# Kernel optimization log

Hardware: AMD Instinct MI355X
Metric: run time of the kernel (lower is better)

Reference implementation:

```python
import jax, jax.numpy as jnp
import numpy as np

EPS = 1e-10

def _iou(a, b):
    """IoU for boxes in (cx, cy, w, h) format; a, b: (..., 4)."""
    a_min = a[..., :2] - a[..., 2:] * 0.5
    a_max = a[..., :2] + a[..., 2:] * 0.5
    b_min = b[..., :2] - b[..., 2:] * 0.5
    b_max = b[..., :2] + b[..., 2:] * 0.5
    inter_wh = jnp.clip(jnp.minimum(a_max, b_max) - jnp.maximum(a_min, b_min), 0.0)
    inter = inter_wh[..., 0] * inter_wh[..., 1]
    area_a = a[..., 2] * a[..., 3]
    area_b = b[..., 2] * b[..., 3]
    return inter / (area_a + area_b - inter + EPS)

def setup_inputs() -> dict:
    key = jax.random.key(0)
    k1, k2, k3 = jax.random.split(key, 3)
    BATCH, S, C = 16384, 7, 30
    # uniform in (0.01, 1) so sqrt() of w,h channels is finite/differentiable
    preds = jax.random.uniform(k1, (BATCH, S, S, C), jnp.float32, 0.01, 1.0)
    labels = jax.random.uniform(k2, (BATCH, S, S, C), jnp.float32, 0.01, 1.0)
    obj = jax.random.bernoulli(k3, 0.15, (BATCH, S, S)).astype(jnp.float32)
    labels = labels.at[..., 4].set(obj)  # code branches on labels[...,4] == 1
    return {"preds": preds, "labels": labels}

def reference(preds, labels):
    batch = preds.shape[0]
    obj = labels[..., 4] == 1.0  # (B, S, S)
    # faithful quirk: label bbox x-coord is read transposed (labels[i, y, x, 0])
    lb0 = jnp.swapaxes(labels[..., 0], 1, 2)
    lbox = jnp.stack([lb0, labels[..., 1], labels[..., 2], labels[..., 3]], axis=-1)
    iou1 = _iou(preds[..., 0:4], lbox)
    iou2 = _iou(preds[..., 5:9], lbox)
    choose1 = iou1 > iou2
    # branch where box 1 is responsible
    b1 = (5.0 * jnp.sum((preds[..., 0:2] - labels[..., 0:2]) ** 2, -1)
          + jnp.sum((jnp.sqrt(preds[..., 2:4]) - jnp.sqrt(labels[..., 2:4])) ** 2, -1)
          + (iou1 - preds[..., 4]) ** 2
          + 0.5 * preds[..., 9] ** 2)
    # branch where box 2 is responsible (targets read from labels[...,5:9] as in source)
    b2 = (5.0 * jnp.sum((preds[..., 5:7] - labels[..., 5:7]) ** 2, -1)
          + jnp.sum((jnp.sqrt(preds[..., 7:9]) - jnp.sqrt(labels[..., 7:9])) ** 2, -1)
          + (iou2 - preds[..., 9]) ** 2
          + 0.5 * preds[..., 4] ** 2)
    cls = jnp.sum((labels[..., 10:] - preds[..., 10:]) ** 2, -1)
    obj_loss = jnp.where(choose1, b1, b2) + cls
    noobj_loss = 0.5 * (preds[..., 4] ** 2 + preds[..., 9] ** 2)
    total = jnp.sum(jnp.where(obj, obj_loss, noobj_loss))
    return total / batch
```

## Files before the change

kernel.cpp:

```cpp
#include <hip/hip_runtime.h>


#define BATCH 16384
#define S 7
#define C 30
#define NCELLS (BATCH * S * S)
#define BLOCK 256
#define NC 256
#define NBLK (NCELLS / NC)
#define F4_PER_ARR (NC * C / 4)

#define GLOBAL_LOAD_LDS16(g, l)                                         \
    __builtin_amdgcn_global_load_lds(                                   \
        (const __attribute__((address_space(1))) void*)(g),             \
        (__attribute__((address_space(3))) void*)(l), 16, 0, 0)

__device__ __forceinline__ float sq(float v) { return v * v; }

__device__ __forceinline__ float iou_box(float acx, float acy, float aw, float ah,
                                         float bcx, float bcy, float bw, float bh) {
    float ax0 = acx - aw * 0.5f, ax1 = acx + aw * 0.5f;
    float ay0 = acy - ah * 0.5f, ay1 = acy + ah * 0.5f;
    float bx0 = bcx - bw * 0.5f, bx1 = bcx + bw * 0.5f;
    float by0 = bcy - bh * 0.5f, by1 = bcy + bh * 0.5f;
    float iw = fmaxf(fminf(ax1, bx1) - fmaxf(ax0, bx0), 0.0f);
    float ih = fmaxf(fminf(ay1, by1) - fmaxf(ay0, by0), 0.0f);
    float inter = iw * ih;
    float denom = aw * ah + bw * bh - inter + 1e-10f;
    return inter / denom;
}

__global__ __launch_bounds__(BLOCK) void yolo_partial_kernel(
        const float* __restrict__ preds,
        const float* __restrict__ labels,
        float* __restrict__ partials) {
    __shared__ __align__(16) float sp[NC * C];
    __shared__ __align__(16) float sl[NC * C];

    const int tid  = threadIdx.x;
    const int lane = tid & 63;
    const int wv   = tid >> 6;
    const int base_cell = blockIdx.x * NC;

    const float4* gp = reinterpret_cast<const float4*>(preds  + (size_t)base_cell * C);
    const float4* gl = reinterpret_cast<const float4*>(labels + (size_t)base_cell * C);

    #pragma unroll
    for (int k = 0; k < 7; ++k) {
        int f4 = k * 256 + wv * 64;
        GLOBAL_LOAD_LDS16(gp + f4 + lane, (char*)sp + (size_t)f4 * 16);
        GLOBAL_LOAD_LDS16(gl + f4 + lane, (char*)sl + (size_t)f4 * 16);
    }
    if (wv < 2) {
        int f4 = 1792 + wv * 64;
        GLOBAL_LOAD_LDS16(gp + f4 + lane, (char*)sp + (size_t)f4 * 16);
    } else {
        int f4 = 1792 + (wv - 2) * 64;
        GLOBAL_LOAD_LDS16(gl + f4 + lane, (char*)sl + (size_t)f4 * 16);
    }
    __syncthreads();

    const float* p = sp + tid * C;
    const float* l = sl + tid * C;
    float pv[C], lv[C];
    #pragma unroll
    for (int i = 0; i < C / 2; ++i) {
        float2 tp = *reinterpret_cast<const float2*>(p + 2 * i);
        pv[2 * i] = tp.x; pv[2 * i + 1] = tp.y;
        float2 tl = *reinterpret_cast<const float2*>(l + 2 * i);
        lv[2 * i] = tl.x; lv[2 * i + 1] = tl.y;
    }

    int cell = base_cell + tid;
    int b    = cell / (S * S);
    int rem  = cell - b * (S * S);
    int y    = rem / S;
    int x    = rem - y * S;
    int pc   = b * (S * S) + x * S + y;
    float lb0;
    if (pc >= base_cell && pc < base_cell + NC) {
        lb0 = sl[(pc - base_cell) * C];
    } else {
        lb0 = labels[(size_t)pc * C];
    }

    float iou1 = iou_box(pv[0], pv[1], pv[2], pv[3], lb0, lv[1], lv[2], lv[3]);
    float iou2 = iou_box(pv[5], pv[6], pv[7], pv[8], lb0, lv[1], lv[2], lv[3]);

    float b1 = 5.0f * (sq(pv[0] - lv[0]) + sq(pv[1] - lv[1]))
             + sq(sqrtf(pv[2]) - sqrtf(lv[2])) + sq(sqrtf(pv[3]) - sqrtf(lv[3]))
             + sq(iou1 - pv[4])
             + 0.5f * pv[9] * pv[9];

    float b2 = 5.0f * (sq(pv[5] - lv[5]) + sq(pv[6] - lv[6]))
             + sq(sqrtf(pv[7]) - sqrtf(lv[7])) + sq(sqrtf(pv[8]) - sqrtf(lv[8]))
             + sq(iou2 - pv[9])
             + 0.5f * pv[4] * pv[4];

    float cls = 0.0f;
    #pragma unroll
    for (int c = 10; c < C; ++c) cls += sq(lv[c] - pv[c]);

    float obj_loss   = ((iou1 > iou2) ? b1 : b2) + cls;
    float noobj_loss = 0.5f * (pv[4] * pv[4] + pv[9] * pv[9]);
    float loss = (lv[4] == 1.0f) ? obj_loss : noobj_loss;

    #pragma unroll
    for (int off = 32; off > 0; off >>= 1)
        loss += __shfl_down(loss, off, 64);

    __shared__ float wsum[BLOCK / 64];
    if (lane == 0) wsum[wv] = loss;
    __syncthreads();
    if (tid == 0) {
        partials[blockIdx.x] = wsum[0] + wsum[1] + wsum[2] + wsum[3];
    }
}

__global__ __launch_bounds__(BLOCK) void yolo_reduce_kernel(
        const float* __restrict__ partials,
        float* __restrict__ out) {
    const int tid = threadIdx.x;
    float s = 0.0f;
    for (int i = tid; i < NBLK; i += BLOCK) s += partials[i];

    #pragma unroll
    for (int off = 32; off > 0; off >>= 1)
        s += __shfl_down(s, off, 64);

    __shared__ float wsum[BLOCK / 64];
    int lane = tid & 63;
    int wv   = tid >> 6;
    if (lane == 0) wsum[wv] = s;
    __syncthreads();
    if (tid == 0) {
        out[0] = (wsum[0] + wsum[1] + wsum[2] + wsum[3]) * (1.0f / (float)BATCH);
    }
}

extern "C" void kernel_launch(void* const* d_in, const int* in_sizes, int n_in,
                              void* d_out, int out_size, void* d_ws, size_t ws_size,
                              hipStream_t stream) {
    const float* preds  = (const float*)d_in[0];
    const float* labels = (const float*)d_in[1];
    float* out = (float*)d_out;
    float* partials = (float*)d_ws;

    yolo_partial_kernel<<<NBLK, BLOCK, 0, stream>>>(preds, labels, partials);
    yolo_reduce_kernel<<<1, BLOCK, 0, stream>>>(partials, out);
}
```

Before: 206.1 us.

## Replace LDS staging with direct per-thread float2 global loads

Drops the global_load_lds staging of preds and labels into shared memory and has each thread read its own 30-float cell straight from global memory with float2 loads, plus an occupancy hint in launch_bounds. This removes the LDS buffers, the block barrier and the shared-memory reads, which should allow more resident blocks per CU. In exchange each thread reads with a 120-byte stride, so accesses are poorly coalesced within a wavefront and depend on cache lines being reused across lanes, and the transposed lb0 read now always goes to global memory.

```diff
diff --git a/kernel.cpp b/kernel.cpp
--- a/kernel.cpp
+++ b/kernel.cpp
@@ -6,16 +6,13 @@
 #define C 30
 #define NCELLS (BATCH * S * S)
 #define BLOCK 256
-#define NC 256
-#define NBLK (NCELLS / NC)
-#define F4_PER_ARR (NC * C / 4)
-
-#define GLOBAL_LOAD_LDS16(g, l)                                         \
-    __builtin_amdgcn_global_load_lds(                                   \
-        (const __attribute__((address_space(1))) void*)(g),             \
-        (__attribute__((address_space(3))) void*)(l), 16, 0, 0)
+#define NBLK (NCELLS / BLOCK)
 
 __device__ __forceinline__ float sq(float v) { return v * v; }
+
+__device__ __forceinline__ float2 ld2(const float* a) {
+    return *reinterpret_cast<const float2*>(a);
+}
 
 __device__ __forceinline__ float iou_box(float acx, float acy, float aw, float ah,
                                          float bcx, float bcy, float bw, float bh) {
@@ -30,86 +27,60 @@
     return inter / denom;
 }
 
-__global__ __launch_bounds__(BLOCK) void yolo_partial_kernel(
+__global__ __launch_bounds__(BLOCK, 4) void yolo_partial_kernel(
         const float* __restrict__ preds,
         const float* __restrict__ labels,
         float* __restrict__ partials) {
-    __shared__ __align__(16) float sp[NC * C];
-    __shared__ __align__(16) float sl[NC * C];
+    const int tid  = threadIdx.x;
+    const int cell = blockIdx.x * BLOCK + tid;
 
-    const int tid  = threadIdx.x;
-    const int lane = tid & 63;
-    const int wv   = tid >> 6;
-    const int base_cell = blockIdx.x * NC;
+    const float* p = preds  + (size_t)cell * C;
+    const float* l = labels + (size_t)cell * C;
 
-    const float4* gp = reinterpret_cast<const float4*>(preds  + (size_t)base_cell * C);
-    const float4* gl = reinterpret_cast<const float4*>(labels + (size_t)base_cell * C);
+    const int b   = cell / (S * S);
+    const int rem = cell - b * (S * S);
+    const int y   = rem / S;
+    const int x   = rem - y * S;
+    const int pc  = b * (S * S) + x * S + y;
+    const float lb0 = labels[(size_t)pc * C];
 
-    #pragma unroll
-    for (int k = 0; k < 7; ++k) {
-        int f4 = k * 256 + wv * 64;
-        GLOBAL_LOAD_LDS16(gp + f4 + lane, (char*)sp + (size_t)f4 * 16);
-        GLOBAL_LOAD_LDS16(gl + f4 + lane, (char*)sl + (size_t)f4 * 16);
-    }
-    if (wv < 2) {
-        int f4 = 1792 + wv * 64;
-        GLOBAL_LOAD_LDS16(gp + f4 + lane, (char*)sp + (size_t)f4 * 16);
-    } else {
-        int f4 = 1792 + (wv - 2) * 64;
-        GLOBAL_LOAD_LDS16(gl + f4 + lane, (char*)sl + (size_t)f4 * 16);
-    }
-    __syncthreads();
-
-    const float* p = sp + tid * C;
-    const float* l = sl + tid * C;
-    float pv[C], lv[C];
-    #pragma unroll
-    for (int i = 0; i < C / 2; ++i) {
-        float2 tp = *reinterpret_cast<const float2*>(p + 2 * i);
-        pv[2 * i] = tp.x; pv[2 * i + 1] = tp.y;
-        float2 tl = *reinterpret_cast<const float2*>(l + 2 * i);
-        lv[2 * i] = tl.x; lv[2 * i + 1] = tl.y;
-    }
-
-    int cell = base_cell + tid;
-    int b    = cell / (S * S);
-    int rem  = cell - b * (S * S);
-    int y    = rem / S;
-    int x    = rem - y * S;
-    int pc   = b * (S * S) + x * S + y;
-    float lb0;
-    if (pc >= base_cell && pc < base_cell + NC) {
-        lb0 = sl[(pc - base_cell) * C];
-    } else {
-        lb0 = labels[(size_t)pc * C];
-    }
-
-    float iou1 = iou_box(pv[0], pv[1], pv[2], pv[3], lb0, lv[1], lv[2], lv[3]);
-    float iou2 = iou_box(pv[5], pv[6], pv[7], pv[8], lb0, lv[1], lv[2], lv[3]);
-
-    float b1 = 5.0f * (sq(pv[0] - lv[0]) + sq(pv[1] - lv[1]))
-             + sq(sqrtf(pv[2]) - sqrtf(lv[2])) + sq(sqrtf(pv[3]) - sqrtf(lv[3]))
-             + sq(iou1 - pv[4])
-             + 0.5f * pv[9] * pv[9];
-
-    float b2 = 5.0f * (sq(pv[5] - lv[5]) + sq(pv[6] - lv[6]))
-             + sq(sqrtf(pv[7]) - sqrtf(lv[7])) + sq(sqrtf(pv[8]) - sqrtf(lv[8]))
-             + sq(iou2 - pv[9])
-             + 0.5f * pv[4] * pv[4];
+    float2 p01 = ld2(p + 0), p23 = ld2(p + 2), p45 = ld2(p + 4),
+           p67 = ld2(p + 6), p89 = ld2(p + 8);
+    float2 l01 = ld2(l + 0), l23 = ld2(l + 2), l45 = ld2(l + 4),
+           l67 = ld2(l + 6), l89 = ld2(l + 8);
 
     float cls = 0.0f;
     #pragma unroll
-    for (int c = 10; c < C; ++c) cls += sq(lv[c] - pv[c]);
+    for (int c = 10; c < C; c += 2) {
+        float2 tp = ld2(p + c);
+        float2 tl = ld2(l + c);
+        cls += sq(tl.x - tp.x) + sq(tl.y - tp.y);
+    }
+
+    float iou1 = iou_box(p01.x, p01.y, p23.x, p23.y, lb0, l01.y, l23.x, l23.y);
+    float iou2 = iou_box(p45.y, p67.x, p67.y, p89.x, lb0, l01.y, l23.x, l23.y);
+
+    float b1 = 5.0f * (sq(p01.x - l01.x) + sq(p01.y - l01.y))
+             + sq(sqrtf(p23.x) - sqrtf(l23.x)) + sq(sqrtf(p23.y) - sqrtf(l23.y))
+             + sq(iou1 - p45.x)
+             + 0.5f * p89.y * p89.y;
+
+    float b2 = 5.0f * (sq(p45.y - l45.y) + sq(p67.x - l67.x))
+             + sq(sqrtf(p67.y) - sqrtf(l67.y)) + sq(sqrtf(p89.x) - sqrtf(l89.x))
+             + sq(iou2 - p89.y)
+             + 0.5f * p45.x * p45.x;
 
     float obj_loss   = ((iou1 > iou2) ? b1 : b2) + cls;
-    float noobj_loss = 0.5f * (pv[4] * pv[4] + pv[9] * pv[9]);
-    float loss = (lv[4] == 1.0f) ? obj_loss : noobj_loss;
+    float noobj_loss = 0.5f * (p45.x * p45.x + p89.y * p89.y);
+    float loss = (l45.x == 1.0f) ? obj_loss : noobj_loss;
 
     #pragma unroll
     for (int off = 32; off > 0; off >>= 1)
         loss += __shfl_down(loss, off, 64);
 
     __shared__ float wsum[BLOCK / 64];
+    const int lane = tid & 63;
+    const int wv   = tid >> 6;
     if (lane == 0) wsum[wv] = loss;
     __syncthreads();
     if (tid == 0) {
```

Measured after the change: 209.2 us. About the same (+1.5%).

## Use single-wave blocks looping over four 64-cell tiles with small LDS

Applied to the files above, without the earlier changes.

Restructures the partial kernel into 64-thread blocks that process four 64-cell tiles sequentially, each staged into a compact shared-memory layout of about 16 KB instead of 60 KB. The label tail and pred tail chunks are loaded together into one overlap region, then the pred tail is copied into place. The aim is to raise occupancy by cutting LDS per block, at the cost of an extra copy, three barriers per tile and loads that are serialised within a block. The transposed label x-coordinate is now always read from global memory.

```diff
diff --git a/kernel.cpp b/kernel.cpp
--- a/kernel.cpp
+++ b/kernel.cpp
@@ -5,10 +5,16 @@
 #define S 7
 #define C 30
 #define NCELLS (BATCH * S * S)
-#define BLOCK 256
-#define NC 256
-#define NBLK (NCELLS / NC)
-#define F4_PER_ARR (NC * C / 4)
+#define BLOCK 64
+#define TILES 4
+#define CELLS_PER_TILE 64
+#define CELLS_PER_BLOCK (TILES * CELLS_PER_TILE)
+#define NBLK (NCELLS / CELLS_PER_BLOCK)
+
+#define SL_OFF   0
+#define TAILP_OFF 1920
+#define SP_OFF   2048
+#define LDS_FLOATS 3968
 
 #define GLOBAL_LOAD_LDS16(g, l)                                         \
     __builtin_amdgcn_global_load_lds(                                   \
@@ -34,101 +40,102 @@
         const float* __restrict__ preds,
         const float* __restrict__ labels,
         float* __restrict__ partials) {
-    __shared__ __align__(16) float sp[NC * C];
-    __shared__ __align__(16) float sl[NC * C];
+    __shared__ __align__(16) float lds[LDS_FLOATS];
 
-    const int tid  = threadIdx.x;
-    const int lane = tid & 63;
-    const int wv   = tid >> 6;
-    const int base_cell = blockIdx.x * NC;
-
-    const float4* gp = reinterpret_cast<const float4*>(preds  + (size_t)base_cell * C);
-    const float4* gl = reinterpret_cast<const float4*>(labels + (size_t)base_cell * C);
+    const int tid = threadIdx.x;
+    float tsum[TILES];
 
     #pragma unroll
-    for (int k = 0; k < 7; ++k) {
-        int f4 = k * 256 + wv * 64;
-        GLOBAL_LOAD_LDS16(gp + f4 + lane, (char*)sp + (size_t)f4 * 16);
-        GLOBAL_LOAD_LDS16(gl + f4 + lane, (char*)sl + (size_t)f4 * 16);
-    }
-    if (wv < 2) {
-        int f4 = 1792 + wv * 64;
-        GLOBAL_LOAD_LDS16(gp + f4 + lane, (char*)sp + (size_t)f4 * 16);
-    } else {
-        int f4 = 1792 + (wv - 2) * 64;
-        GLOBAL_LOAD_LDS16(gl + f4 + lane, (char*)sl + (size_t)f4 * 16);
-    }
-    __syncthreads();
+    for (int t = 0; t < TILES; ++t) {
+        const int base_cell = blockIdx.x * CELLS_PER_BLOCK + t * CELLS_PER_TILE;
+        const float4* gp = reinterpret_cast<const float4*>(preds  + (size_t)base_cell * C);
+        const float4* gl = reinterpret_cast<const float4*>(labels + (size_t)base_cell * C);
 
-    const float* p = sp + tid * C;
-    const float* l = sl + tid * C;
-    float pv[C], lv[C];
-    #pragma unroll
-    for (int i = 0; i < C / 2; ++i) {
-        float2 tp = *reinterpret_cast<const float2*>(p + 2 * i);
-        pv[2 * i] = tp.x; pv[2 * i + 1] = tp.y;
-        float2 tl = *reinterpret_cast<const float2*>(l + 2 * i);
-        lv[2 * i] = tl.x; lv[2 * i + 1] = tl.y;
+        __syncthreads();
+
+        #pragma unroll
+        for (int k = 0; k < 7; ++k)
+            GLOBAL_LOAD_LDS16(gl + k * 64 + tid, (char*)lds + (size_t)k * 1024);
+        #pragma unroll
+        for (int k = 0; k < 7; ++k)
+            GLOBAL_LOAD_LDS16(gp + k * 64 + tid,
+                              (char*)lds + (size_t)SP_OFF * 4 + (size_t)k * 1024);
+        {
+            const float4* src = (tid < 32) ? (gl + 448 + tid) : (gp + 448 + (tid - 32));
+            GLOBAL_LOAD_LDS16(src, (char*)lds + 7168);
+        }
+
+        const int cell = base_cell + tid;
+        const int b    = cell / (S * S);
+        const int rem  = cell - b * (S * S);
+        const int y    = rem / S;
+        const int x    = rem - y * S;
+        const int pc   = b * (S * S) + x * S + y;
+        const float lb0 = labels[(size_t)pc * C];
+
+        __syncthreads();
+
+        {
+            float2 v = *reinterpret_cast<const float2*>(&lds[TAILP_OFF + 2 * tid]);
+            *reinterpret_cast<float2*>(&lds[SP_OFF + 1792 + 2 * tid]) = v;
+        }
+        __syncthreads();
+
+        const float* p = &lds[SP_OFF + tid * C];
+        const float* l = &lds[SL_OFF + tid * C];
+        float pv[C], lv[C];
+        #pragma unroll
+        for (int i = 0; i < C / 2; ++i) {
+            float2 tp = *reinterpret_cast<const float2*>(p + 2 * i);
+            pv[2 * i] = tp.x; pv[2 * i + 1] = tp.y;
+            float2 tl = *reinterpret_cast<const float2*>(l + 2 * i);
+            lv[2 * i] = tl.x; lv[2 * i + 1] = tl.y;
+        }
+
+        float iou1 = iou_box(pv[0], pv[1], pv[2], pv[3], lb0, lv[1], lv[2], lv[3]);
+        float iou2 = iou_box(pv[5], pv[6], pv[7], pv[8], lb0, lv[1], lv[2], lv[3]);
+
+        float b1 = 5.0f * (sq(pv[0] - lv[0]) + sq(pv[1] - lv[1]))
+                 + sq(sqrtf(pv[2]) - sqrtf(lv[2])) + sq(sqrtf(pv[3]) - sqrtf(lv[3]))
+                 + sq(iou1 - pv[4])
+                 + 0.5f * pv[9] * pv[9];
+
+        float b2 = 5.0f * (sq(pv[5] - lv[5]) + sq(pv[6] - lv[6]))
+                 + sq(sqrtf(pv[7]) - sqrtf(lv[7])) + sq(sqrtf(pv[8]) - sqrtf(lv[8]))
+                 + sq(iou2 - pv[9])
+                 + 0.5f * pv[4] * pv[4];
+
+        float cls = 0.0f;
+        #pragma unroll
+        for (int c = 10; c < C; ++c) cls += sq(lv[c] - pv[c]);
+
+        float obj_loss   = ((iou1 > iou2) ? b1 : b2) + cls;
+        float noobj_loss = 0.5f * (pv[4] * pv[4] + pv[9] * pv[9]);
+        float loss = (lv[4] == 1.0f) ? obj_loss : noobj_loss;
+
+        #pragma unroll
+        for (int off = 32; off > 0; off >>= 1)
+            loss += __shfl_down(loss, off, 64);
+        tsum[t] = loss;
     }
 
-    int cell = base_cell + tid;
-    int b    = cell / (S * S);
-    int rem  = cell - b * (S * S);
-    int y    = rem / S;
-    int x    = rem - y * S;
-    int pc   = b * (S * S) + x * S + y;
-    float lb0;
-    if (pc >= base_cell && pc < base_cell + NC) {
-        lb0 = sl[(pc - base_cell) * C];
-    } else {
-        lb0 = labels[(size_t)pc * C];
-    }
-
-    float iou1 = iou_box(pv[0], pv[1], pv[2], pv[3], lb0, lv[1], lv[2], lv[3]);
-    float iou2 = iou_box(pv[5], pv[6], pv[7], pv[8], lb0, lv[1], lv[2], lv[3]);
-
-    float b1 = 5.0f * (sq(pv[0] - lv[0]) + sq(pv[1] - lv[1]))
-             + sq(sqrtf(pv[2]) - sqrtf(lv[2])) + sq(sqrtf(pv[3]) - sqrtf(lv[3]))
-             + sq(iou1 - pv[4])
-             + 0.5f * pv[9] * pv[9];
-
-    float b2 = 5.0f * (sq(pv[5] - lv[5]) + sq(pv[6] - lv[6]))
-             + sq(sqrtf(pv[7]) - sqrtf(lv[7])) + sq(sqrtf(pv[8]) - sqrtf(lv[8]))
-             + sq(iou2 - pv[9])
-             + 0.5f * pv[4] * pv[4];
-
-    float cls = 0.0f;
-    #pragma unroll
-    for (int c = 10; c < C; ++c) cls += sq(lv[c] - pv[c]);
-
-    float obj_loss   = ((iou1 > iou2) ? b1 : b2) + cls;
-    float noobj_loss = 0.5f * (pv[4] * pv[4] + pv[9] * pv[9]);
-    float loss = (lv[4] == 1.0f) ? obj_loss : noobj_loss;
-
-    #pragma unroll
-    for (int off = 32; off > 0; off >>= 1)
-        loss += __shfl_down(loss, off, 64);
-
-    __shared__ float wsum[BLOCK / 64];
-    if (lane == 0) wsum[wv] = loss;
-    __syncthreads();
     if (tid == 0) {
-        partials[blockIdx.x] = wsum[0] + wsum[1] + wsum[2] + wsum[3];
+        partials[blockIdx.x] = ((tsum[0] + tsum[1]) + tsum[2]) + tsum[3];
     }
 }
 
-__global__ __launch_bounds__(BLOCK) void yolo_reduce_kernel(
+__global__ __launch_bounds__(256) void yolo_reduce_kernel(
         const float* __restrict__ partials,
         float* __restrict__ out) {
     const int tid = threadIdx.x;
     float s = 0.0f;
-    for (int i = tid; i < NBLK; i += BLOCK) s += partials[i];
+    for (int i = tid; i < NBLK; i += 256) s += partials[i];
 
     #pragma unroll
     for (int off = 32; off > 0; off >>= 1)
         s += __shfl_down(s, off, 64);
 
-    __shared__ float wsum[BLOCK / 64];
+    __shared__ float wsum[4];
     int lane = tid & 63;
     int wv   = tid >> 6;
     if (lane == 0) wsum[wv] = s;
@@ -147,5 +154,5 @@
     float* partials = (float*)d_ws;
 
     yolo_partial_kernel<<<NBLK, BLOCK, 0, stream>>>(preds, labels, partials);
-    yolo_reduce_kernel<<<1, BLOCK, 0, stream>>>(partials, out);
+    yolo_reduce_kernel<<<1, 256, 0, stream>>>(partials, out);
 }
```

Result: slower. 214.4 us (+4.0%).
